# Kernel optimization log

Measured on AMD Instinct MI355X. Metric: run time of the kernel, lower is better.

Reference implementation:

```python
import jax, jax.numpy as jnp
import numpy as np
from jax import lax

N_FEATURES = 160
HIDDEN = 128
NUM_LAYERS = 2
BATCH = 256
SEQ = 512


def _lstm_layer(x, h0, c0, W_ih, W_hh, b_ih, b_hh):
    """Single LSTM layer, batch_first input x: [B, T, D]. Returns hs: [B, T, H].
    PyTorch gate order: i, f, g, o."""
    b = b_ih + b_hh  # [4H]

    def step(carry, xt):
        h, c = carry
        gates = xt @ W_ih.T + h @ W_hh.T + b  # [B, 4H]
        i, f, g, o = jnp.split(gates, 4, axis=-1)
        i = jax.nn.sigmoid(i)
        f = jax.nn.sigmoid(f)
        g = jnp.tanh(g)
        o = jax.nn.sigmoid(o)
        c = f * c + i * g
        h = o * jnp.tanh(c)
        return (h, c), h

    xs = jnp.swapaxes(x, 0, 1)  # [T, B, D]
    (_, _), hs = lax.scan(step, (h0, c0), xs)
    return jnp.swapaxes(hs, 0, 1)  # [B, T, H]


def setup_inputs() -> dict:
    key = jax.random.key(0)
    ks = jax.random.split(key, 9)
    s = 1.0 / np.sqrt(HIDDEN)  # PyTorch LSTM init scale
    x = jax.random.normal(ks[0], (BATCH, SEQ, N_FEATURES), dtype=jnp.float32)
    h0 = jnp.zeros((NUM_LAYERS, BATCH, HIDDEN), dtype=jnp.float32)
    c0 = jnp.zeros((NUM_LAYERS, BATCH, HIDDEN), dtype=jnp.float32)
    return {
        "x": x,
        "h0": h0,
        "c0": c0,
        "W_ih0": jax.random.uniform(ks[1], (4 * HIDDEN, N_FEATURES), jnp.float32, -s, s),
        "W_hh0": jax.random.uniform(ks[2], (4 * HIDDEN, HIDDEN), jnp.float32, -s, s),
        "b_ih0": jax.random.uniform(ks[3], (4 * HIDDEN,), jnp.float32, -s, s),
        "b_hh0": jax.random.uniform(ks[4], (4 * HIDDEN,), jnp.float32, -s, s),
        "W_ih1": jax.random.uniform(ks[5], (4 * HIDDEN, HIDDEN), jnp.float32, -s, s),
        "W_hh1": jax.random.uniform(ks[6], (4 * HIDDEN, HIDDEN), jnp.float32, -s, s),
        "b_ih1": jax.random.uniform(ks[7], (4 * HIDDEN,), jnp.float32, -s, s),
        "b_hh1": jax.random.uniform(ks[8], (4 * HIDDEN,), jnp.float32, -s, s),
    }


def reference(x, h0, c0, W_ih0, W_hh0, b_ih0, b_hh0, W_ih1, W_hh1, b_ih1, b_hh1):
    h1 = _lstm_layer(x, h0[0], c0[0], W_ih0, W_hh0, b_ih0, b_hh0)   # [B, T, H]
    h2 = _lstm_layer(h1, h0[1], c0[1], W_ih1, W_hh1, b_ih1, b_hh1)  # [B, T, H]
    return h2[:, -1:, :]  # [B, 1, H]
```

## Files before the change

kernel.cpp:

```cpp
#include <hip/hip_runtime.h>


typedef _Float16 half2_t __attribute__((ext_vector_type(2)));

#define T_STEPS 512
#define HID     128
#define NGATES  512

static __device__ __forceinline__ unsigned pack2(float a, float b) {
  half2_t h;
  h[0] = (_Float16)a;
  h[1] = (_Float16)b;
  return __builtin_bit_cast(unsigned, h);
}

static __device__ __forceinline__ float dot2f(unsigned a, unsigned b, float c) {
#if __has_builtin(__builtin_amdgcn_fdot2)
  return __builtin_amdgcn_fdot2(__builtin_bit_cast(half2_t, a),
                                __builtin_bit_cast(half2_t, b), c, false);
#else
  half2_t x = __builtin_bit_cast(half2_t, a);
  half2_t y = __builtin_bit_cast(half2_t, b);
  float r = c;
  r = fmaf((float)x[0], (float)y[0], r);
  r = fmaf((float)x[1], (float)y[1], r);
  return r;
#endif
}

static __device__ __forceinline__ float fast_rcp(float x) {
#if __has_builtin(__builtin_amdgcn_rcpf)
  return __builtin_amdgcn_rcpf(x);
#else
  return 1.0f / x;
#endif
}

static __device__ __forceinline__ float fast_exp2(float x) {
#if __has_builtin(__builtin_amdgcn_exp2f)
  return __builtin_amdgcn_exp2f(x);
#else
  return exp2f(x);
#endif
}

static __device__ __forceinline__ float sigm(float x) {
  return fast_rcp(1.0f + fast_exp2(x * -1.44269504f));
}
static __device__ __forceinline__ float tanh_f(float x) {
  float e = fast_exp2(x * 2.885390082f);
  return 1.0f - 2.0f * fast_rcp(e + 1.0f);
}

__global__ __launch_bounds__(512, 1) void lstm_fused(
    const float* __restrict__ x,
    const float* __restrict__ h0,
    const float* __restrict__ c0,
    const float* __restrict__ Wih0,
    const float* __restrict__ Whh0,
    const float* __restrict__ bih0, const float* __restrict__ bhh0,
    const float* __restrict__ Wih1,
    const float* __restrict__ Whh1,
    const float* __restrict__ bih1, const float* __restrict__ bhh1,
    float* __restrict__ out)
{
  const int b = blockIdx.x;
  const int n = threadIdx.x;

  __shared__ unsigned h1s[T_STEPS * 64];
  __shared__ unsigned xbuf[80];
  __shared__ unsigned hbuf[64];
  __shared__ float glds[NGATES];

  {
    unsigned wih[80];
    unsigned whh[64];
#pragma unroll
    for (int j = 0; j < 80; ++j)
      wih[j] = pack2(Wih0[n * 160 + 2 * j], Wih0[n * 160 + 2 * j + 1]);
#pragma unroll
    for (int j = 0; j < 64; ++j)
      whh[j] = pack2(Whh0[n * HID + 2 * j], Whh0[n * HID + 2 * j + 1]);
    const float bias = bih0[n] + bhh0[n];

    float c = 0.0f;
    if (n < HID) c = c0[b * HID + n];
    if (n < 64) hbuf[n] = pack2(h0[b * HID + 2 * n], h0[b * HID + 2 * n + 1]);

    float2 xr = make_float2(0.f, 0.f);
    if (n < 80) xr = *(const float2*)&x[((long long)b * T_STEPS + 0) * 160 + 2 * n];

#pragma unroll 1
    for (int t = 0; t < T_STEPS; ++t) {
      if (n < 80) xbuf[n] = pack2(xr.x, xr.y);
      __syncthreads();

      if (n < 80) {
        int tn = (t + 1 < T_STEPS) ? t + 1 : t;
        xr = *(const float2*)&x[((long long)b * T_STEPS + tn) * 160 + 2 * n];
      }

      float a0 = bias, a1 = 0.f, a2 = 0.f, a3 = 0.f;
      const uint4* xb4 = (const uint4*)xbuf;
#pragma unroll
      for (int j = 0; j < 20; ++j) {
        uint4 v = xb4[j];
        a0 = dot2f(v.x, wih[4 * j + 0], a0);
        a1 = dot2f(v.y, wih[4 * j + 1], a1);
        a2 = dot2f(v.z, wih[4 * j + 2], a2);
        a3 = dot2f(v.w, wih[4 * j + 3], a3);
      }
      const uint4* hb4 = (const uint4*)hbuf;
#pragma unroll
      for (int j = 0; j < 16; ++j) {
        uint4 v = hb4[j];
        a0 = dot2f(v.x, whh[4 * j + 0], a0);
        a1 = dot2f(v.y, whh[4 * j + 1], a1);
        a2 = dot2f(v.z, whh[4 * j + 2], a2);
        a3 = dot2f(v.w, whh[4 * j + 3], a3);
      }
      glds[n] = (a0 + a1) + (a2 + a3);
      __syncthreads();

      if (n < HID) {
        float iv = sigm(glds[n]);
        float fv = sigm(glds[HID + n]);
        float gv = tanh_f(glds[2 * HID + n]);
        float ov = sigm(glds[3 * HID + n]);
        c = fv * c + iv * gv;
        float h = ov * tanh_f(c);
        _Float16 hf = (_Float16)h;
        reinterpret_cast<_Float16*>(hbuf)[n] = hf;
        reinterpret_cast<_Float16*>(h1s)[t * HID + n] = hf;
      }
    }
  }

  {
    __syncthreads();

    unsigned wih[64];
    unsigned whh[64];
#pragma unroll
    for (int j = 0; j < 64; ++j)
      wih[j] = pack2(Wih1[n * HID + 2 * j], Wih1[n * HID + 2 * j + 1]);
#pragma unroll
    for (int j = 0; j < 64; ++j)
      whh[j] = pack2(Whh1[n * HID + 2 * j], Whh1[n * HID + 2 * j + 1]);
    const float bias = bih1[n] + bhh1[n];

    const float* h0b = h0 + 256 * HID;
    const float* c0b = c0 + 256 * HID;
    float c = 0.0f;
    if (n < HID) c = c0b[b * HID + n];
    if (n < 64) hbuf[n] = pack2(h0b[b * HID + 2 * n], h0b[b * HID + 2 * n + 1]);

#pragma unroll 1
    for (int t = 0; t < T_STEPS; ++t) {
      __syncthreads();

      float a0 = bias, a1 = 0.f, a2 = 0.f, a3 = 0.f;
      const uint4* xb4 = (const uint4*)(h1s + t * 64);
#pragma unroll
      for (int j = 0; j < 16; ++j) {
        uint4 v = xb4[j];
        a0 = dot2f(v.x, wih[4 * j + 0], a0);
        a1 = dot2f(v.y, wih[4 * j + 1], a1);
        a2 = dot2f(v.z, wih[4 * j + 2], a2);
        a3 = dot2f(v.w, wih[4 * j + 3], a3);
      }
      const uint4* hb4 = (const uint4*)hbuf;
#pragma unroll
      for (int j = 0; j < 16; ++j) {
        uint4 v = hb4[j];
        a0 = dot2f(v.x, whh[4 * j + 0], a0);
        a1 = dot2f(v.y, whh[4 * j + 1], a1);
        a2 = dot2f(v.z, whh[4 * j + 2], a2);
        a3 = dot2f(v.w, whh[4 * j + 3], a3);
      }
      glds[n] = (a0 + a1) + (a2 + a3);
      __syncthreads();

      if (n < HID) {
        float iv = sigm(glds[n]);
        float fv = sigm(glds[HID + n]);
        float gv = tanh_f(glds[2 * HID + n]);
        float ov = sigm(glds[3 * HID + n]);
        c = fv * c + iv * gv;
        float h = ov * tanh_f(c);
        reinterpret_cast<_Float16*>(hbuf)[n] = (_Float16)h;
        if (t == T_STEPS - 1) out[b * HID + n] = h;
      }
    }
  }
}

extern "C" void kernel_launch(void* const* d_in, const int* in_sizes, int n_in,
                              void* d_out, int out_size, void* d_ws,
                              size_t ws_size, hipStream_t stream) {
  const float* x    = (const float*)d_in[0];
  const float* h0   = (const float*)d_in[1];
  const float* c0   = (const float*)d_in[2];
  const float* Wih0 = (const float*)d_in[3];
  const float* Whh0 = (const float*)d_in[4];
  const float* bih0 = (const float*)d_in[5];
  const float* bhh0 = (const float*)d_in[6];
  const float* Wih1 = (const float*)d_in[7];
  const float* Whh1 = (const float*)d_in[8];
  const float* bih1 = (const float*)d_in[9];
  const float* bhh1 = (const float*)d_in[10];

  lstm_fused<<<256, 512, 0, stream>>>(x, h0, c0, Wih0, Whh0, bih0, bhh0,
                                      Wih1, Whh1, bih1, bhh1, (float*)d_out);
}
```

Measured before the change: 1.081 ms.

## Split gate dot products across 1024 threads with DPP reduction, one sync per step

Each hidden unit is now handled by 8 threads: 4 split the reduction dimension and 2 each own two of the four gates. Partial sums are combined with DPP quad adds and gates are exchanged with ds_swizzle, so the gate LDS buffer and the second barrier per step go away. The x and h buffers are double-buffered, and layer 0 reads h straight from the h1s history. This shortens each thread's serial dot-product chain and cuts per-step synchronisation, in exchange for twice the threads per block, more cross-lane operations, and a tanh computed through a scaled sigmoid.

Result: slower. 1.126 ms (+4.2%).

```diff
diff --git a/kernel.cpp b/kernel.cpp
--- a/kernel.cpp
+++ b/kernel.cpp
@@ -3,14 +3,11 @@
 
 typedef _Float16 half2_t __attribute__((ext_vector_type(2)));
 
-#define T_STEPS 512
-#define HID     128
-#define NGATES  512
+#define TSTEPS 512
+#define HID 128
 
 static __device__ __forceinline__ unsigned pack2(float a, float b) {
-  half2_t h;
-  h[0] = (_Float16)a;
-  h[1] = (_Float16)b;
+  half2_t h; h[0] = (_Float16)a; h[1] = (_Float16)b;
   return __builtin_bit_cast(unsigned, h);
 }
 
@@ -35,7 +32,6 @@
   return 1.0f / x;
 #endif
 }
-
 static __device__ __forceinline__ float fast_exp2(float x) {
 #if __has_builtin(__builtin_amdgcn_exp2f)
   return __builtin_amdgcn_exp2f(x);
@@ -43,7 +39,6 @@
   return exp2f(x);
 #endif
 }
-
 static __device__ __forceinline__ float sigm(float x) {
   return fast_rcp(1.0f + fast_exp2(x * -1.44269504f));
 }
@@ -52,7 +47,18 @@
   return 1.0f - 2.0f * fast_rcp(e + 1.0f);
 }
 
-__global__ __launch_bounds__(512, 1) void lstm_fused(
+template <int CTRL>
+static __device__ __forceinline__ float qp_add(float v) {
+  int iv = __builtin_bit_cast(int, v);
+  int t = __builtin_amdgcn_update_dpp(iv, iv, CTRL, 0xF, 0xF, true);
+  return v + __builtin_bit_cast(float, t);
+}
+static __device__ __forceinline__ float swz_xor4(float v) {
+  int t = __builtin_amdgcn_ds_swizzle(__builtin_bit_cast(int, v), 0x101F);
+  return __builtin_bit_cast(float, t);
+}
+
+__global__ __launch_bounds__(1024, 1) void lstm_fused(
     const float* __restrict__ x,
     const float* __restrict__ h0,
     const float* __restrict__ c0,
@@ -64,134 +70,185 @@
     const float* __restrict__ bih1, const float* __restrict__ bhh1,
     float* __restrict__ out)
 {
-  const int b = blockIdx.x;
-  const int n = threadIdx.x;
-
-  __shared__ unsigned h1s[T_STEPS * 64];
-  __shared__ unsigned xbuf[80];
-  __shared__ unsigned hbuf[64];
-  __shared__ float glds[NGATES];
+  const int b  = blockIdx.x;
+  const int tid = threadIdx.x;
+  const int c  = tid >> 3;
+  const int tp = (tid >> 2) & 1;
+  const int s  = tid & 3;
+
+  __shared__ unsigned h1s[TSTEPS][64];
+  __shared__ unsigned xbuf[2][96];
+  __shared__ unsigned h0buf[64];
+  __shared__ unsigned hbuf[2][64];
 
   {
-    unsigned wih[80];
-    unsigned whh[64];
-#pragma unroll
-    for (int j = 0; j < 80; ++j)
-      wih[j] = pack2(Wih0[n * 160 + 2 * j], Wih0[n * 160 + 2 * j + 1]);
-#pragma unroll
-    for (int j = 0; j < 64; ++j)
-      whh[j] = pack2(Whh0[n * HID + 2 * j], Whh0[n * HID + 2 * j + 1]);
-    const float bias = bih0[n] + bhh0[n];
-
-    float c = 0.0f;
-    if (n < HID) c = c0[b * HID + n];
-    if (n < 64) hbuf[n] = pack2(h0[b * HID + 2 * n], h0[b * HID + 2 * n + 1]);
-
-    float2 xr = make_float2(0.f, 0.f);
-    if (n < 80) xr = *(const float2*)&x[((long long)b * T_STEPS + 0) * 160 + 2 * n];
+    unsigned wx[2][24], wh[2][16];
+    float bias[2];
+#pragma unroll
+    for (int u = 0; u < 2; ++u) {
+      const int r = (tp * 2 + u) * HID + c;
+#pragma unroll
+      for (int j = 0; j < 24; ++j) {
+        int p = 24 * s + j;
+        float a0 = (2 * p < 160) ? Wih0[r * 160 + 2 * p] : 0.f;
+        float a1 = (2 * p + 1 < 160) ? Wih0[r * 160 + 2 * p + 1] : 0.f;
+        wx[u][j] = pack2(a0, a1);
+      }
+#pragma unroll
+      for (int j = 0; j < 16; ++j) {
+        int p = 16 * s + j;
+        wh[u][j] = pack2(Whh0[r * HID + 2 * p], Whh0[r * HID + 2 * p + 1]);
+      }
+      bias[u] = bih0[r] + bhh0[r];
+    }
+
+    float cst = c0[b * HID + c];
+
+    if (tid < 64) h0buf[tid] = pack2(h0[b * HID + 2 * tid], h0[b * HID + 2 * tid + 1]);
+    if (tid < 80) {
+      float2 v = *(const float2*)&x[((size_t)b * TSTEPS + 0) * 160 + 2 * tid];
+      xbuf[0][tid] = pack2(v.x, v.y);
+    }
+    if (tid >= 80 && tid < 96) { xbuf[0][tid] = 0u; xbuf[1][tid] = 0u; }
+    float2 xA = make_float2(0.f, 0.f);
+    if (tid < 80) xA = *(const float2*)&x[((size_t)b * TSTEPS + 1) * 160 + 2 * tid];
+    __syncthreads();
 
 #pragma unroll 1
-    for (int t = 0; t < T_STEPS; ++t) {
-      if (n < 80) xbuf[n] = pack2(xr.x, xr.y);
+    for (int t = 0; t < TSTEPS; ++t) {
+      float2 xB = xA;
+      if (tid < 80) {
+        int tn = (t + 2 < TSTEPS) ? t + 2 : TSTEPS - 1;
+        xB = *(const float2*)&x[((size_t)b * TSTEPS + tn) * 160 + 2 * tid];
+      }
+
+      const uint4* xs = (const uint4*)&xbuf[t & 1][24 * s];
+      const uint4* hs = (t == 0) ? (const uint4*)&h0buf[16 * s]
+                                 : (const uint4*)&h1s[t - 1][16 * s];
+      float a0 = 0.f, a1 = 0.f, b0 = 0.f, b1 = 0.f;
+#pragma unroll
+      for (int k = 0; k < 6; ++k) {
+        uint4 v = xs[k];
+        a0 = dot2f(v.x, wx[0][4 * k + 0], a0);
+        a0 = dot2f(v.y, wx[0][4 * k + 1], a0);
+        a1 = dot2f(v.z, wx[0][4 * k + 2], a1);
+        a1 = dot2f(v.w, wx[0][4 * k + 3], a1);
+        b0 = dot2f(v.x, wx[1][4 * k + 0], b0);
+        b0 = dot2f(v.y, wx[1][4 * k + 1], b0);
+        b1 = dot2f(v.z, wx[1][4 * k + 2], b1);
+        b1 = dot2f(v.w, wx[1][4 * k + 3], b1);
+      }
+#pragma unroll
+      for (int k = 0; k < 4; ++k) {
+        uint4 v = hs[k];
+        a0 = dot2f(v.x, wh[0][4 * k + 0], a0);
+        a0 = dot2f(v.y, wh[0][4 * k + 1], a0);
+        a1 = dot2f(v.z, wh[0][4 * k + 2], a1);
+        a1 = dot2f(v.w, wh[0][4 * k + 3], a1);
+        b0 = dot2f(v.x, wh[1][4 * k + 0], b0);
+        b0 = dot2f(v.y, wh[1][4 * k + 1], b0);
+        b1 = dot2f(v.z, wh[1][4 * k + 2], b1);
+        b1 = dot2f(v.w, wh[1][4 * k + 3], b1);
+      }
+      float accA = a0 + a1, accB = b0 + b1;
+      accA = qp_add<0xB1>(accA); accA = qp_add<0x4E>(accA);
+      accB = qp_add<0xB1>(accB); accB = qp_add<0x4E>(accB);
+      float g0 = accA + bias[0];
+      float g1 = accB + bias[1];
+      float m = tp ? 2.0f : 1.0f;
+      float act0 = m * sigm(m * g0) - (tp ? 1.0f : 0.0f);
+      float act1 = sigm(g1);
+      float e0 = swz_xor4(act0);
+      float e1 = swz_xor4(act1);
+      float ih = tp ? e0 : act0;
+      float fh = tp ? e1 : act1;
+      float gh = tp ? act0 : e0;
+      float oh = tp ? act1 : e1;
+      cst = fh * cst + ih * gh;
+      float h = oh * tanh_f(cst);
+
+      if ((tid & 7) == 0)
+        ((_Float16*)h1s)[t * HID + c] = (_Float16)h;
+      if (tid < 80) xbuf[(t + 1) & 1][tid] = pack2(xA.x, xA.y);
       __syncthreads();
-
-      if (n < 80) {
-        int tn = (t + 1 < T_STEPS) ? t + 1 : t;
-        xr = *(const float2*)&x[((long long)b * T_STEPS + tn) * 160 + 2 * n];
-      }
-
-      float a0 = bias, a1 = 0.f, a2 = 0.f, a3 = 0.f;
-      const uint4* xb4 = (const uint4*)xbuf;
-#pragma unroll
-      for (int j = 0; j < 20; ++j) {
-        uint4 v = xb4[j];
-        a0 = dot2f(v.x, wih[4 * j + 0], a0);
-        a1 = dot2f(v.y, wih[4 * j + 1], a1);
-        a2 = dot2f(v.z, wih[4 * j + 2], a2);
-        a3 = dot2f(v.w, wih[4 * j + 3], a3);
-      }
-      const uint4* hb4 = (const uint4*)hbuf;
+      xA = xB;
+    }
+  }
+
+  {
+    unsigned w1x[2][16], w1h[2][16];
+    float bias[2];
+#pragma unroll
+    for (int u = 0; u < 2; ++u) {
+      const int r = (tp * 2 + u) * HID + c;
 #pragma unroll
       for (int j = 0; j < 16; ++j) {
-        uint4 v = hb4[j];
-        a0 = dot2f(v.x, whh[4 * j + 0], a0);
-        a1 = dot2f(v.y, whh[4 * j + 1], a1);
-        a2 = dot2f(v.z, whh[4 * j + 2], a2);
-        a3 = dot2f(v.w, whh[4 * j + 3], a3);
-      }
-      glds[n] = (a0 + a1) + (a2 + a3);
-      __syncthreads();
-
-      if (n < HID) {
-        float iv = sigm(glds[n]);
-        float fv = sigm(glds[HID + n]);
-        float gv = tanh_f(glds[2 * HID + n]);
-        float ov = sigm(glds[3 * HID + n]);
-        c = fv * c + iv * gv;
-        float h = ov * tanh_f(c);
-        _Float16 hf = (_Float16)h;
-        reinterpret_cast<_Float16*>(hbuf)[n] = hf;
-        reinterpret_cast<_Float16*>(h1s)[t * HID + n] = hf;
-      }
-    }
-  }
-
-  {
-    __syncthreads();
-
-    unsigned wih[64];
-    unsigned whh[64];
-#pragma unroll
-    for (int j = 0; j < 64; ++j)
-      wih[j] = pack2(Wih1[n * HID + 2 * j], Wih1[n * HID + 2 * j + 1]);
-#pragma unroll
-    for (int j = 0; j < 64; ++j)
-      whh[j] = pack2(Whh1[n * HID + 2 * j], Whh1[n * HID + 2 * j + 1]);
-    const float bias = bih1[n] + bhh1[n];
+        int p = 16 * s + j;
+        w1x[u][j] = pack2(Wih1[r * HID + 2 * p], Wih1[r * HID + 2 * p + 1]);
+        w1h[u][j] = pack2(Whh1[r * HID + 2 * p], Whh1[r * HID + 2 * p + 1]);
+      }
+      bias[u] = bih1[r] + bhh1[r];
+    }
 
     const float* h0b = h0 + 256 * HID;
     const float* c0b = c0 + 256 * HID;
-    float c = 0.0f;
-    if (n < HID) c = c0b[b * HID + n];
-    if (n < 64) hbuf[n] = pack2(h0b[b * HID + 2 * n], h0b[b * HID + 2 * n + 1]);
-
+    float cst = c0b[b * HID + c];
+    if (tid < 64) hbuf[0][tid] = pack2(h0b[b * HID + 2 * tid], h0b[b * HID + 2 * tid + 1]);
+    __syncthreads();
+
+    float hlast = 0.f;
 #pragma unroll 1
-    for (int t = 0; t < T_STEPS; ++t) {
+    for (int t = 0; t < TSTEPS; ++t) {
+      const uint4* xs = (const uint4*)&h1s[t][16 * s];
+      const uint4* hs = (const uint4*)&hbuf[t & 1][16 * s];
+      float a0 = 0.f, a1 = 0.f, b0 = 0.f, b1 = 0.f;
+#pragma unroll
+      for (int k = 0; k < 4; ++k) {
+        uint4 v = xs[k];
+        a0 = dot2f(v.x, w1x[0][4 * k + 0], a0);
+        a0 = dot2f(v.y, w1x[0][4 * k + 1], a0);
+        a1 = dot2f(v.z, w1x[0][4 * k + 2], a1);
+        a1 = dot2f(v.w, w1x[0][4 * k + 3], a1);
+        b0 = dot2f(v.x, w1x[1][4 * k + 0], b0);
+        b0 = dot2f(v.y, w1x[1][4 * k + 1], b0);
+        b1 = dot2f(v.z, w1x[1][4 * k + 2], b1);
+        b1 = dot2f(v.w, w1x[1][4 * k + 3], b1);
+      }
+#pragma unroll
+      for (int k = 0; k < 4; ++k) {
+        uint4 v = hs[k];
+        a0 = dot2f(v.x, w1h[0][4 * k + 0], a0);
+        a0 = dot2f(v.y, w1h[0][4 * k + 1], a0);
+        a1 = dot2f(v.z, w1h[0][4 * k + 2], a1);
+        a1 = dot2f(v.w, w1h[0][4 * k + 3], a1);
+        b0 = dot2f(v.x, w1h[1][4 * k + 0], b0);
+        b0 = dot2f(v.y, w1h[1][4 * k + 1], b0);
+        b1 = dot2f(v.z, w1h[1][4 * k + 2], b1);
+        b1 = dot2f(v.w, w1h[1][4 * k + 3], b1);
+      }
+      float accA = a0 + a1, accB = b0 + b1;
+      accA = qp_add<0xB1>(accA); accA = qp_add<0x4E>(accA);
+      accB = qp_add<0xB1>(accB); accB = qp_add<0x4E>(accB);
+      float g0 = accA + bias[0];
+      float g1 = accB + bias[1];
+      float m = tp ? 2.0f : 1.0f;
+      float act0 = m * sigm(m * g0) - (tp ? 1.0f : 0.0f);
+      float act1 = sigm(g1);
+      float e0 = swz_xor4(act0);
+      float e1 = swz_xor4(act1);
+      float ih = tp ? e0 : act0;
+      float fh = tp ? e1 : act1;
+      float gh = tp ? act0 : e0;
+      float oh = tp ? act1 : e1;
+      cst = fh * cst + ih * gh;
+      float h = oh * tanh_f(cst);
+      hlast = h;
+
+      if ((tid & 7) == 0)
+        ((_Float16*)hbuf)[(((t + 1) & 1) * 64) * 2 + c] = (_Float16)h;
       __syncthreads();
-
-      float a0 = bias, a1 = 0.f, a2 = 0.f, a3 = 0.f;
-      const uint4* xb4 = (const uint4*)(h1s + t * 64);
-#pragma unroll
-      for (int j = 0; j < 16; ++j) {
-        uint4 v = xb4[j];
-        a0 = dot2f(v.x, wih[4 * j + 0], a0);
-        a1 = dot2f(v.y, wih[4 * j + 1], a1);
-        a2 = dot2f(v.z, wih[4 * j + 2], a2);
-        a3 = dot2f(v.w, wih[4 * j + 3], a3);
-      }
-      const uint4* hb4 = (const uint4*)hbuf;
-#pragma unroll
-      for (int j = 0; j < 16; ++j) {
-        uint4 v = hb4[j];
-        a0 = dot2f(v.x, whh[4 * j + 0], a0);
-        a1 = dot2f(v.y, whh[4 * j + 1], a1);
-        a2 = dot2f(v.z, whh[4 * j + 2], a2);
-        a3 = dot2f(v.w, whh[4 * j + 3], a3);
-      }
-      glds[n] = (a0 + a1) + (a2 + a3);
-      __syncthreads();
-
-      if (n < HID) {
-        float iv = sigm(glds[n]);
-        float fv = sigm(glds[HID + n]);
-        float gv = tanh_f(glds[2 * HID + n]);
-        float ov = sigm(glds[3 * HID + n]);
-        c = fv * c + iv * gv;
-        float h = ov * tanh_f(c);
-        reinterpret_cast<_Float16*>(hbuf)[n] = (_Float16)h;
-        if (t == T_STEPS - 1) out[b * HID + n] = h;
-      }
-    }
+    }
+    if ((tid & 7) == 0) out[b * HID + c] = hlast;
   }
 }
 
@@ -210,6 +267,6 @@
   const float* bih1 = (const float*)d_in[9];
   const float* bhh1 = (const float*)d_in[10];
 
-  lstm_fused<<<256, 512, 0, stream>>>(x, h0, c0, Wih0, Whh0, bih0, bhh0,
-                                      Wih1, Whh1, bih1, bhh1, (float*)d_out);
-}
+  lstm_fused<<<256, 1024, 0, stream>>>(x, h0, c0, Wih0, Whh0, bih0, bhh0,
+                                       Wih1, Whh1, bih1, bhh1, (float*)d_out);
+}
```
